# Kernel optimization log

Measured on AMD Instinct MI355X. Metric: run time of the kernel, lower is better.

## Reference

```python
import jax, jax.numpy as jnp
import numpy as np


def _wn(v, g):
    # weight norm over input axis: w[:, j] = g[j] * v[:, j] / ||v[:, j]||
    norm = jnp.sqrt(jnp.sum(v * v, axis=0, keepdims=True))
    return v * (g[None, :] / norm)


def setup_inputs() -> dict:
    key = jax.random.key(0)
    ks = jax.random.split(key, 6)
    M, K1, H, OUT = 65536, 512, 1024, 512
    x = jax.random.normal(ks[0], (M, K1), dtype=jnp.float32)
    v1 = jax.random.normal(ks[1], (K1, H), dtype=jnp.float32) * 0.05
    v2 = jax.random.normal(ks[2], (H, H), dtype=jnp.float32) * 0.05
    v3 = jax.random.normal(ks[3], (H, H), dtype=jnp.float32) * 0.05
    v4 = jax.random.normal(ks[4], (H, H), dtype=jnp.float32) * 0.05
    v5 = jax.random.normal(ks[5], (H, OUT), dtype=jnp.float32) * 0.05
    g1 = jnp.ones((H,), jnp.float32)
    g2 = jnp.ones((H,), jnp.float32)
    g3 = jnp.ones((H,), jnp.float32)
    g4 = jnp.ones((H,), jnp.float32)
    g5 = jnp.ones((OUT,), jnp.float32)
    return {"x": x, "v1": v1, "g1": g1, "v2": v2, "g2": g2,
            "v3": v3, "g3": g3, "v4": v4, "g4": g4, "v5": v5, "g5": g5}


def reference(x, v1, g1, v2, g2, v3, g3, v4, g4, v5, g5):
    w1 = _wn(v1, g1)
    w2 = _wn(v2, g2)
    w3 = _wn(v3, g3)
    w4 = _wn(v4, g4)
    w5 = _wn(v5, g5)
    h1 = jax.nn.softplus(x @ w1)    # [M, H]
    h2 = jax.nn.softplus(h1 @ w2)
    h3 = jax.nn.softplus(h2 @ w3)
    h4 = jax.nn.softplus(h3 @ w4)
    out = h4 @ w5                   # final layer linear
    return out
```

## Files before the change

kernel.cpp:

```cpp
#include <hip/hip_runtime.h>
#include <hip/hip_bf16.h>
#include <cstdint>

typedef unsigned short u16;
typedef __attribute__((ext_vector_type(8))) _Float16 f16x8;
typedef __attribute__((ext_vector_type(4))) float f32x4;
typedef __attribute__((ext_vector_type(8))) unsigned short u16x8;

typedef const __attribute__((address_space(1))) void* gas1p;
typedef __attribute__((address_space(3))) void* las3p;

__device__ __forceinline__ void gld_lds16(const void* g, void* l) {
    __builtin_amdgcn_global_load_lds((gas1p)g, (las3p)l, 16, 0, 0);
}

__device__ __forceinline__ u16 f2h(float f) {
    _Float16 h = (_Float16)f;
    return __builtin_bit_cast(u16, h);
}

__global__ void cvt_x_kernel(const float4* __restrict__ x, u16* __restrict__ xb) {
    size_t i = (size_t)blockIdx.x * blockDim.x + threadIdx.x;
    float4 a = x[2 * i];
    float4 b = x[2 * i + 1];
    u16x8 o;
    o[0] = f2h(a.x); o[1] = f2h(a.y); o[2] = f2h(a.z); o[3] = f2h(a.w);
    o[4] = f2h(b.x); o[5] = f2h(b.y); o[6] = f2h(b.z); o[7] = f2h(b.w);
    *(u16x8*)&xb[i * 8] = o;
}

struct WnDesc {
    const float* v; const float* g; u16* wT; float* partial;
    int K; int N; int blk0;
};
struct WnPack { WnDesc d[5]; int nlayer; };

__global__ void wn_partial_all(WnPack p) {
    int b = blockIdx.x;
    int l = 0;
    while (l + 1 < p.nlayer && b >= p.d[l + 1].blk0) l++;
    const WnDesc& d = p.d[l];
    int lb = b - d.blk0;
    int nbx = d.N >> 6;
    int bx = lb % nbx, seg = lb / nbx;

    int lane = threadIdx.x & 63;
    int tr = threadIdx.x >> 6;
    int n = bx * 64 + lane;
    int kseg = d.K >> 3;
    int kbeg = seg * kseg;
    float s = 0.f;
    for (int k = kbeg + tr; k < kbeg + kseg; k += 4) {
        float x = d.v[(size_t)k * d.N + n];
        s += x * x;
    }
    __shared__ float red[4][64];
    red[tr][lane] = s;
    __syncthreads();
    if (tr == 0)
        d.partial[seg * d.N + n] = red[0][lane] + red[1][lane] + red[2][lane] + red[3][lane];
}

__global__ void wn_write_all(WnPack p) {
    int b = blockIdx.x;
    int l = 0;
    while (l + 1 < p.nlayer && b >= p.d[l + 1].blk0) l++;
    const WnDesc& d = p.d[l];
    int lb = b - d.blk0;
    int nbx = d.N >> 6;
    int bx = lb % nbx, seg = lb / nbx;

    int lane = threadIdx.x & 63;
    int tr = threadIdx.x >> 6;
    int n = bx * 64 + lane;
    float s = 0.f;
#pragma unroll
    for (int i = 0; i < 8; i++) s += d.partial[i * d.N + n];
    float sc = d.g[n] / sqrtf(s);

    int kseg = d.K >> 3;
    int kbeg = seg * kseg;
    for (int k = kbeg + tr; k < kbeg + kseg; k += 4)
        d.wT[(size_t)n * d.K + k] = f2h(d.v[(size_t)k * d.N + n] * sc);
}

template<int N, int K, bool ACT, bool OUTF32>
__global__ __launch_bounds__(512, 2) void gemm_mlp(
    const u16* __restrict__ A, const u16* __restrict__ Bt,
    u16* __restrict__ Ch, float* __restrict__ Cf)
{
    constexpr int M = 65536;
    constexpr int NT = K / 64;
    constexpr int NTN = N / 256;
    constexpr int NWG = (M / 256) * NTN;

    __shared__ u16 sA[2][256 * 64];
    __shared__ u16 sB[2][2 * 128 * 64];

    const int bid = blockIdx.x;
    const int wk = (bid & 7) * (NWG >> 3) + (bid >> 3);
    const int tm = wk / NTN, tn = wk % NTN;
    const long m0 = (long)tm * 256;
    const int n0 = tn * 256;

    const int tid = threadIdx.x;
    const int lane = tid & 63;
    const int wid = tid >> 6;
    const int wm = (wid >> 2) * 128;
    const int wn = (wid & 3) * 64;

    const int r8 = tid >> 3;
    const int gcol = ((tid & 7) ^ (r8 & 7)) * 8;
    const u16* Abase = A + (m0 + r8) * (size_t)K + gcol;
    const u16* Bbase = Bt + (size_t)(n0 + ((r8 >> 5) * 64 + (r8 & 31))) * K + gcol;
    const int dst8 = tid * 8;

    const u16* Aq0 = Abase;
    const u16* Aq1 = Abase + (size_t)64 * K;
    const u16* Aq2 = Abase + (size_t)128 * K;
    const u16* Aq3 = Abase + (size_t)192 * K;
    const u16* B00 = Bbase;
    const u16* B01 = Bbase + (size_t)128 * K;
    const u16* B10 = Bbase + (size_t)32 * K;
    const u16* B11 = Bbase + (size_t)160 * K;

    auto stA = [&](int buf, const u16* base, int t, int q) {
        gld_lds16(base + (size_t)t * 64, &sA[buf][q * 4096 + dst8]);
    };
    auto stB = [&](int buf, const u16* base, int t, int s, int c) {
        gld_lds16(base + (size_t)t * 64, &sB[buf][s * 8192 + c * 4096 + dst8]);
    };

    const int rbase = lane & 15;
    const int co0 = ((lane >> 4) ^ (lane & 7)) * 8;
    const int arow0 = (wm + rbase) * 64 + co0;
    const int brow0 = ((wn >> 6) * 32 + rbase) * 64 + co0;

    f32x4 acc[8][4] = {};
    f16x8 a[4][2], bq[2][2][2];

    auto ldA = [&](int buf, int qm) {
#pragma unroll
        for (int i = 0; i < 4; i++) {
            int base = arow0 + (qm * 64 + i * 16) * 64;
            a[i][0] = *(const f16x8*)&sA[buf][base];
            a[i][1] = *(const f16x8*)&sA[buf][base ^ 32];
        }
    };
    auto ldB = [&](int buf, int qn) {
#pragma unroll
        for (int j2 = 0; j2 < 2; j2++) {
            int base = brow0 + qn * 8192 + j2 * 1024;
            bq[qn][j2][0] = *(const f16x8*)&sB[buf][base];
            bq[qn][j2][1] = *(const f16x8*)&sB[buf][base ^ 32];
        }
    };
    auto mmaq = [&](int qm, int qn) {
        __builtin_amdgcn_s_setprio(1);
#pragma unroll
        for (int kk = 0; kk < 2; kk++)
#pragma unroll
            for (int i = 0; i < 4; i++)
#pragma unroll
                for (int j2 = 0; j2 < 2; j2++)
                    acc[qm * 4 + i][qn * 2 + j2] = __builtin_amdgcn_mfma_f32_16x16x32_f16(
                        a[i][kk], bq[qn][j2][kk], acc[qm * 4 + i][qn * 2 + j2], 0, 0, 0);
        __builtin_amdgcn_s_setprio(0);
    };
    auto bar = [&]() {
        asm volatile("" ::: "memory");
        __builtin_amdgcn_s_barrier();
        asm volatile("" ::: "memory");
    };

    stA(0, Aq0, 0, 0); stA(0, Aq2, 0, 2);
    stB(0, B00, 0, 0, 0); stB(0, B01, 0, 0, 1);
    stB(0, B10, 0, 1, 0); stB(0, B11, 0, 1, 1);
    stA(0, Aq1, 0, 1); stA(0, Aq3, 0, 3);
    stA(1, Aq0, 1, 0); stA(1, Aq2, 1, 2);
    asm volatile("s_waitcnt vmcnt(2)" ::: "memory");
    bar();

#pragma unroll 2
    for (int t = 0; t < NT - 2; t++) {
        const int cur = t & 1, nxt = cur ^ 1;
        stA(nxt, Aq1, t + 1, 1); stA(nxt, Aq3, t + 1, 3);
        ldA(cur, 0); ldB(cur, 0);
        bar();
        mmaq(0, 0);
        stB(nxt, B00, t + 1, 0, 0); stB(nxt, B01, t + 1, 0, 1);
        ldB(cur, 1);
        bar();
        mmaq(0, 1);
        stB(nxt, B10, t + 1, 1, 0); stB(nxt, B11, t + 1, 1, 1);
        ldA(cur, 1);
        bar();
        mmaq(1, 0);
        stA(cur, Aq0, t + 2, 0); stA(cur, Aq2, t + 2, 2);
        asm volatile("s_waitcnt vmcnt(2)" ::: "memory");
        bar();
        mmaq(1, 1);
    }
    {
        const int t = NT - 2, cur = t & 1, nxt = cur ^ 1;
        stA(nxt, Aq1, t + 1, 1); stA(nxt, Aq3, t + 1, 3);
        ldA(cur, 0); ldB(cur, 0);
        bar();
        mmaq(0, 0);
        stB(nxt, B00, t + 1, 0, 0); stB(nxt, B01, t + 1, 0, 1);
        ldB(cur, 1);
        bar();
        mmaq(0, 1);
        stB(nxt, B10, t + 1, 1, 0); stB(nxt, B11, t + 1, 1, 1);
        ldA(cur, 1);
        bar();
        mmaq(1, 0);
        asm volatile("s_waitcnt vmcnt(0)" ::: "memory");
        bar();
        mmaq(1, 1);
    }
    {
        const int cur = (NT - 1) & 1;
        ldA(cur, 0); ldB(cur, 0);
        mmaq(0, 0);
        ldB(cur, 1);
        mmaq(0, 1);
        ldA(cur, 1);
        mmaq(1, 0);
        mmaq(1, 1);
    }

    const long crow0 = m0 + wm + ((lane >> 4) << 2);
    const int ccol0 = n0 + wn + (lane & 15);
#pragma unroll
    for (int fi = 0; fi < 8; fi++) {
#pragma unroll
        for (int r = 0; r < 4; r++) {
            const size_t rowoff = (size_t)(crow0 + fi * 16 + r) * N;
#pragma unroll
            for (int fj = 0; fj < 4; fj++) {
                float v = acc[fi][fj][r];
                if (ACT) v = fmaxf(v, 0.f) + __logf(1.f + __expf(-fabsf(v)));
                if (OUTF32) Cf[rowoff + ccol0 + fj * 16] = v;
                else        Ch[rowoff + ccol0 + fj * 16] = f2h(v);
            }
        }
    }
}

extern "C" void kernel_launch(void* const* d_in, const int* in_sizes, int n_in,
                              void* d_out, int out_size, void* d_ws, size_t ws_size,
                              hipStream_t stream) {
    const float* x  = (const float*)d_in[0];
    const float* v1 = (const float*)d_in[1];
    const float* g1 = (const float*)d_in[2];
    const float* v2 = (const float*)d_in[3];
    const float* g2 = (const float*)d_in[4];
    const float* v3 = (const float*)d_in[5];
    const float* g3 = (const float*)d_in[6];
    const float* v4 = (const float*)d_in[7];
    const float* g4 = (const float*)d_in[8];
    const float* v5 = (const float*)d_in[9];
    const float* g5 = (const float*)d_in[10];
    float* out = (float*)d_out;

    const int M = 65536;
    char* ws = (char*)d_ws;
    u16* bufA = (u16*)(ws);
    u16* bufB = (u16*)(ws + 0x8000000ULL);
    u16* w1T  = (u16*)(ws + 0x10000000ULL);
    u16* w2T  = w1T + 1024 * 512;
    u16* w3T  = w2T + 1024 * 1024;
    u16* w4T  = w3T + 1024 * 1024;
    u16* w5T  = w4T + 1024 * 1024;
    float* part = (float*)(ws + 0x10800000ULL);

    cvt_x_kernel<<<(M * 512) / (256 * 8), 256, 0, stream>>>((const float4*)x, bufB);

    WnPack pk;
    int cum = 0;
    auto mk = [&](int i, const float* v, const float* g, u16* wT, int K, int N) {
        pk.d[i] = WnDesc{v, g, wT, part + i * 8 * 1024, K, N, cum};
        cum += (N / 64) * 8;
    };
    mk(0, v1, g1, w1T, 512, 1024);
    mk(1, v2, g2, w2T, 1024, 1024);
    mk(2, v3, g3, w3T, 1024, 1024);
    mk(3, v4, g4, w4T, 1024, 1024);
    mk(4, v5, g5, w5T, 1024, 512);
    pk.nlayer = 5;

    wn_partial_all<<<cum, 256, 0, stream>>>(pk);
    wn_write_all<<<cum, 256, 0, stream>>>(pk);

    gemm_mlp<1024, 512,  true,  false><<<1024, 512, 0, stream>>>(bufB, w1T, bufA, nullptr);
    gemm_mlp<1024, 1024, true,  false><<<1024, 512, 0, stream>>>(bufA, w2T, bufB, nullptr);
    gemm_mlp<1024, 1024, true,  false><<<1024, 512, 0, stream>>>(bufB, w3T, bufA, nullptr);
    gemm_mlp<1024, 1024, true,  false><<<1024, 512, 0, stream>>>(bufA, w4T, bufB, nullptr);
    gemm_mlp<512,  1024, false, true ><<<512,  512, 0, stream>>>(bufB, w5T, nullptr, out);

    (void)in_sizes; (void)n_in; (void)out_size; (void)ws_size;
}
```

Baseline: 714.4 us.

## Restructure GEMM main loop into two-tile unrolled pipeline with deeper prefetch

Rewrites the K-loop of the fused MLP GEMM so each iteration processes two K-tiles with fixed buffer indices. The prologue now fills both LDS buffers, and loads of the next tiles are issued in quarter-slices interleaved with the MFMA quarters. The goal is to keep more global-to-LDS loads in flight (vmcnt 4/8 instead of 2) so memory latency is better hidden and per-iteration buffer-index arithmetic disappears. It adds branches on the tail/full flags and changes the waitcnt accounting, which could introduce races if the counts are off.

```diff
diff --git a/kernel.cpp b/kernel.cpp
--- a/kernel.cpp
+++ b/kernel.cpp
@@ -91,6 +91,7 @@
 {
     constexpr int M = 65536;
     constexpr int NT = K / 64;
+    constexpr int J = NT / 2;
     constexpr int NTN = N / 256;
     constexpr int NWG = (M / 256) * NTN;
 
@@ -130,6 +131,10 @@
     auto stB = [&](int buf, const u16* base, int t, int s, int c) {
         gld_lds16(base + (size_t)t * 64, &sB[buf][s * 8192 + c * 4096 + dst8]);
     };
+    auto stA0 = [&](int buf, int t) { stA(buf, Aq0, t, 0); stA(buf, Aq2, t, 2); };
+    auto stA1 = [&](int buf, int t) { stA(buf, Aq1, t, 1); stA(buf, Aq3, t, 3); };
+    auto stB0 = [&](int buf, int t) { stB(buf, B00, t, 0, 0); stB(buf, B01, t, 0, 1); };
+    auto stB1 = [&](int buf, int t) { stB(buf, B10, t, 1, 0); stB(buf, B11, t, 1, 1); };
 
     const int rbase = lane & 15;
     const int co0 = ((lane >> 4) ^ (lane & 7)) * 8;
@@ -173,60 +178,54 @@
         asm volatile("" ::: "memory");
     };
 
-    stA(0, Aq0, 0, 0); stA(0, Aq2, 0, 2);
-    stB(0, B00, 0, 0, 0); stB(0, B01, 0, 0, 1);
-    stB(0, B10, 0, 1, 0); stB(0, B11, 0, 1, 1);
-    stA(0, Aq1, 0, 1); stA(0, Aq3, 0, 3);
-    stA(1, Aq0, 1, 0); stA(1, Aq2, 1, 2);
-    asm volatile("s_waitcnt vmcnt(2)" ::: "memory");
+    stA0(0, 0); stB0(0, 0); stB1(0, 0); stA1(0, 0);
+    stA0(1, 1); stB0(1, 1); stB1(1, 1); stA1(1, 1);
+    asm volatile("s_waitcnt vmcnt(8)" ::: "memory");
     bar();
 
-#pragma unroll 2
-    for (int t = 0; t < NT - 2; t++) {
-        const int cur = t & 1, nxt = cur ^ 1;
-        stA(nxt, Aq1, t + 1, 1); stA(nxt, Aq3, t + 1, 3);
-        ldA(cur, 0); ldB(cur, 0);
+    for (int j = 0; j < J; j++) {
+        const int ta = 2 * j, tb = ta + 1;
+        const bool tail = (j > 0);
+        const bool full = (j + 1 < J);
+
+        if (tail) stB1(1, tb);
+        ldA(0, 0); ldB(0, 0);
         bar();
         mmaq(0, 0);
-        stB(nxt, B00, t + 1, 0, 0); stB(nxt, B01, t + 1, 0, 1);
-        ldB(cur, 1);
+        if (tail) stA1(1, tb);
+        ldB(0, 1);
         bar();
         mmaq(0, 1);
-        stB(nxt, B10, t + 1, 1, 0); stB(nxt, B11, t + 1, 1, 1);
-        ldA(cur, 1);
+        if (full) stA0(0, ta + 2);
+        ldA(0, 1);
         bar();
         mmaq(1, 0);
-        stA(cur, Aq0, t + 2, 0); stA(cur, Aq2, t + 2, 2);
-        asm volatile("s_waitcnt vmcnt(2)" ::: "memory");
+        if (full) {
+            stB0(0, ta + 2);
+            asm volatile("s_waitcnt vmcnt(4)" ::: "memory");
+        } else {
+            asm volatile("s_waitcnt vmcnt(0)" ::: "memory");
+        }
         bar();
         mmaq(1, 1);
-    }
-    {
-        const int t = NT - 2, cur = t & 1, nxt = cur ^ 1;
-        stA(nxt, Aq1, t + 1, 1); stA(nxt, Aq3, t + 1, 3);
-        ldA(cur, 0); ldB(cur, 0);
+
+        if (full) stB1(0, ta + 2);
+        ldA(1, 0); ldB(1, 0);
         bar();
         mmaq(0, 0);
-        stB(nxt, B00, t + 1, 0, 0); stB(nxt, B01, t + 1, 0, 1);
-        ldB(cur, 1);
+        if (full) stA1(0, ta + 2);
+        ldB(1, 1);
         bar();
         mmaq(0, 1);
-        stB(nxt, B10, t + 1, 1, 0); stB(nxt, B11, t + 1, 1, 1);
-        ldA(cur, 1);
+        if (full) stA0(1, tb + 2);
+        ldA(1, 1);
         bar();
         mmaq(1, 0);
-        asm volatile("s_waitcnt vmcnt(0)" ::: "memory");
-        bar();
-        mmaq(1, 1);
-    }
-    {
-        const int cur = (NT - 1) & 1;
-        ldA(cur, 0); ldB(cur, 0);
-        mmaq(0, 0);
-        ldB(cur, 1);
-        mmaq(0, 1);
-        ldA(cur, 1);
-        mmaq(1, 0);
+        if (full) {
+            stB0(1, tb + 2);
+            asm volatile("s_waitcnt vmcnt(4)" ::: "memory");
+            bar();
+        }
         mmaq(1, 1);
     }
 
```

Result: no change. 721.0 us (+0.9%).

## Double-buffer LDS fragment registers and hand-schedule ds_reads with explicit lgkmcnt waits

Applied to the files above, without the earlier changes.

Reworks the GEMM main loop so LDS fragment reads for the next quadrant go into a second set of registers (rA0/rA1, rB0/rB1) while MFMAs run on the current set. Uses inline-asm ds_read_b128 with explicit lgkmcnt waits and sched_barriers, and reorders the global-to-LDS prefetch so a full K-tile is loaded two steps ahead. The goal is to hide LDS read latency behind MFMA work. In exchange it adds more barriers per iteration and extra register pressure, and the hand-set waitcnt values make correctness depend on the exact instruction ordering.

```diff
diff --git a/kernel.cpp b/kernel.cpp
--- a/kernel.cpp
+++ b/kernel.cpp
@@ -9,9 +9,16 @@
 
 typedef const __attribute__((address_space(1))) void* gas1p;
 typedef __attribute__((address_space(3))) void* las3p;
+typedef const __attribute__((address_space(3))) u16* lc16p;
 
 __device__ __forceinline__ void gld_lds16(const void* g, void* l) {
     __builtin_amdgcn_global_load_lds((gas1p)g, (las3p)l, 16, 0, 0);
+}
+
+__device__ __forceinline__ f16x8 dsr128(const u16* p) {
+    f16x8 r;
+    asm volatile("ds_read_b128 %0, %1" : "=v"(r) : "v"((lc16p)p));
+    return r;
 }
 
 __device__ __forceinline__ u16 f2h(float f) {
@@ -115,20 +122,21 @@
     const u16* Bbase = Bt + (size_t)(n0 + ((r8 >> 5) * 64 + (r8 & 31))) * K + gcol;
     const int dst8 = tid * 8;
 
-    const u16* Aq0 = Abase;
-    const u16* Aq1 = Abase + (size_t)64 * K;
-    const u16* Aq2 = Abase + (size_t)128 * K;
-    const u16* Aq3 = Abase + (size_t)192 * K;
-    const u16* B00 = Bbase;
-    const u16* B01 = Bbase + (size_t)128 * K;
-    const u16* B10 = Bbase + (size_t)32 * K;
-    const u16* B11 = Bbase + (size_t)160 * K;
-
-    auto stA = [&](int buf, const u16* base, int t, int q) {
-        gld_lds16(base + (size_t)t * 64, &sA[buf][q * 4096 + dst8]);
-    };
-    auto stB = [&](int buf, const u16* base, int t, int s, int c) {
-        gld_lds16(base + (size_t)t * 64, &sB[buf][s * 8192 + c * 4096 + dst8]);
+    auto stA0 = [&](int buf, int t) {
+        gld_lds16(Abase + (size_t)t * 64, &sA[buf][0 * 4096 + dst8]);
+        gld_lds16(Abase + (size_t)128 * K + (size_t)t * 64, &sA[buf][2 * 4096 + dst8]);
+    };
+    auto stA1 = [&](int buf, int t) {
+        gld_lds16(Abase + (size_t)64 * K + (size_t)t * 64, &sA[buf][1 * 4096 + dst8]);
+        gld_lds16(Abase + (size_t)192 * K + (size_t)t * 64, &sA[buf][3 * 4096 + dst8]);
+    };
+    auto stB0 = [&](int buf, int t) {
+        gld_lds16(Bbase + (size_t)t * 64, &sB[buf][dst8]);
+        gld_lds16(Bbase + (size_t)128 * K + (size_t)t * 64, &sB[buf][4096 + dst8]);
+    };
+    auto stB1 = [&](int buf, int t) {
+        gld_lds16(Bbase + (size_t)32 * K + (size_t)t * 64, &sB[buf][8192 + dst8]);
+        gld_lds16(Bbase + (size_t)160 * K + (size_t)t * 64, &sB[buf][8192 + 4096 + dst8]);
     };
 
     const int rbase = lane & 15;
@@ -137,25 +145,25 @@
     const int brow0 = ((wn >> 6) * 32 + rbase) * 64 + co0;
 
     f32x4 acc[8][4] = {};
-    f16x8 a[4][2], bq[2][2][2];
-
-    auto ldA = [&](int buf, int qm) {
+    f16x8 rA0[4][2], rA1[4][2], rB0[2][2], rB1[2][2];
+
+    auto dsrA = [&](f16x8 (&r)[4][2], int buf, int qm) {
 #pragma unroll
         for (int i = 0; i < 4; i++) {
             int base = arow0 + (qm * 64 + i * 16) * 64;
-            a[i][0] = *(const f16x8*)&sA[buf][base];
-            a[i][1] = *(const f16x8*)&sA[buf][base ^ 32];
+            r[i][0] = dsr128(&sA[buf][base]);
+            r[i][1] = dsr128(&sA[buf][base ^ 32]);
         }
     };
-    auto ldB = [&](int buf, int qn) {
+    auto dsrB = [&](f16x8 (&r)[2][2], int buf, int qn) {
 #pragma unroll
         for (int j2 = 0; j2 < 2; j2++) {
             int base = brow0 + qn * 8192 + j2 * 1024;
-            bq[qn][j2][0] = *(const f16x8*)&sB[buf][base];
-            bq[qn][j2][1] = *(const f16x8*)&sB[buf][base ^ 32];
+            r[j2][0] = dsr128(&sB[buf][base]);
+            r[j2][1] = dsr128(&sB[buf][base ^ 32]);
         }
     };
-    auto mmaq = [&](int qm, int qn) {
+    auto mm = [&](f16x8 (&ra)[4][2], f16x8 (&rb)[2][2], int qm, int qn) {
         __builtin_amdgcn_s_setprio(1);
 #pragma unroll
         for (int kk = 0; kk < 2; kk++)
@@ -164,71 +172,84 @@
 #pragma unroll
                 for (int j2 = 0; j2 < 2; j2++)
                     acc[qm * 4 + i][qn * 2 + j2] = __builtin_amdgcn_mfma_f32_16x16x32_f16(
-                        a[i][kk], bq[qn][j2][kk], acc[qm * 4 + i][qn * 2 + j2], 0, 0, 0);
+                        ra[i][kk], rb[j2][kk], acc[qm * 4 + i][qn * 2 + j2], 0, 0, 0);
         __builtin_amdgcn_s_setprio(0);
     };
-    auto bar = [&]() {
+    auto BAR = [&]() {
         asm volatile("" ::: "memory");
         __builtin_amdgcn_s_barrier();
         asm volatile("" ::: "memory");
     };
-
-    stA(0, Aq0, 0, 0); stA(0, Aq2, 0, 2);
-    stB(0, B00, 0, 0, 0); stB(0, B01, 0, 0, 1);
-    stB(0, B10, 0, 1, 0); stB(0, B11, 0, 1, 1);
-    stA(0, Aq1, 0, 1); stA(0, Aq3, 0, 3);
-    stA(1, Aq0, 1, 0); stA(1, Aq2, 1, 2);
-    asm volatile("s_waitcnt vmcnt(2)" ::: "memory");
-    bar();
-
-#pragma unroll 2
+#define LGKM(n) { asm volatile("s_waitcnt lgkmcnt(" #n ")"); __builtin_amdgcn_sched_barrier(0); }
+
+    stA0(0, 0); stB0(0, 0); stA1(0, 0); stB1(0, 0);
+    stA0(1, 1); stB0(1, 1); stA1(1, 1); stB1(1, 1);
+    asm volatile("s_waitcnt vmcnt(8)" ::: "memory");
+    BAR();
+    dsrA(rA0, 0, 0); dsrB(rB0, 0, 0);
+    LGKM(0);
+    BAR();
+
     for (int t = 0; t < NT - 2; t++) {
         const int cur = t & 1, nxt = cur ^ 1;
-        stA(nxt, Aq1, t + 1, 1); stA(nxt, Aq3, t + 1, 3);
-        ldA(cur, 0); ldB(cur, 0);
-        bar();
-        mmaq(0, 0);
-        stB(nxt, B00, t + 1, 0, 0); stB(nxt, B01, t + 1, 0, 1);
-        ldB(cur, 1);
-        bar();
-        mmaq(0, 1);
-        stB(nxt, B10, t + 1, 1, 0); stB(nxt, B11, t + 1, 1, 1);
-        ldA(cur, 1);
-        bar();
-        mmaq(1, 0);
-        stA(cur, Aq0, t + 2, 0); stA(cur, Aq2, t + 2, 2);
-        asm volatile("s_waitcnt vmcnt(2)" ::: "memory");
-        bar();
-        mmaq(1, 1);
+        dsrB(rB1, cur, 1);
+        stA0(cur, t + 2);
+        BAR(); LGKM(4);
+        mm(rA0, rB0, 0, 0);
+        BAR();
+        dsrA(rA1, cur, 1);
+        stB0(cur, t + 2);
+        BAR(); LGKM(8);
+        mm(rA0, rB1, 0, 1);
+        BAR();
+        asm volatile("s_waitcnt vmcnt(4)" ::: "memory");
+        dsrA(rA0, nxt, 0);
+        BAR(); LGKM(8);
+        mm(rA1, rB0, 1, 0);
+        BAR();
+        dsrB(rB0, nxt, 0);
+        stA1(cur, t + 2); stB1(cur, t + 2);
+        BAR();
+        mm(rA1, rB1, 1, 1);
+        LGKM(4);
+        BAR();
     }
     {
-        const int t = NT - 2, cur = t & 1, nxt = cur ^ 1;
-        stA(nxt, Aq1, t + 1, 1); stA(nxt, Aq3, t + 1, 3);
-        ldA(cur, 0); ldB(cur, 0);
-        bar();
-        mmaq(0, 0);
-        stB(nxt, B00, t + 1, 0, 0); stB(nxt, B01, t + 1, 0, 1);
-        ldB(cur, 1);
-        bar();
-        mmaq(0, 1);
-        stB(nxt, B10, t + 1, 1, 0); stB(nxt, B11, t + 1, 1, 1);
-        ldA(cur, 1);
-        bar();
-        mmaq(1, 0);
+        const int cur = (NT - 2) & 1, nxt = cur ^ 1;
+        dsrB(rB1, cur, 1);
+        BAR(); LGKM(4);
+        mm(rA0, rB0, 0, 0);
+        BAR();
+        dsrA(rA1, cur, 1);
+        BAR(); LGKM(8);
+        mm(rA0, rB1, 0, 1);
+        BAR();
         asm volatile("s_waitcnt vmcnt(0)" ::: "memory");
-        bar();
-        mmaq(1, 1);
+        dsrA(rA0, nxt, 0);
+        BAR(); LGKM(8);
+        mm(rA1, rB0, 1, 0);
+        BAR();
+        dsrB(rB0, nxt, 0);
+        BAR();
+        mm(rA1, rB1, 1, 1);
+        LGKM(4);
+        BAR();
     }
     {
         const int cur = (NT - 1) & 1;
-        ldA(cur, 0); ldB(cur, 0);
-        mmaq(0, 0);
-        ldB(cur, 1);
-        mmaq(0, 1);
-        ldA(cur, 1);
-        mmaq(1, 0);
-        mmaq(1, 1);
-    }
+        dsrB(rB1, cur, 1);
+        BAR(); LGKM(4);
+        mm(rA0, rB0, 0, 0);
+        BAR();
+        dsrA(rA1, cur, 1);
+        BAR(); LGKM(8);
+        mm(rA0, rB1, 0, 1);
+        BAR();
+        LGKM(0);
+        mm(rA1, rB0, 1, 0);
+        mm(rA1, rB1, 1, 1);
+    }
+#undef LGKM
 
     const long crow0 = m0 + wm + ((lane >> 4) << 2);
     const int ccol0 = n0 + wn + (lane & 15);
```

Result: no change. 704.9 us (-1.3%).
